# Optimization experiments

Measured on AMD Instinct MI355X. Metric: run time of the kernel, lower is better.

The kernel has to match this reference:

```python
import jax, jax.numpy as jnp
import numpy as np

L, N, D, DZ = 128, 65536, 8, 16


def setup_inputs() -> dict:
    key = jax.random.key(0)
    k1, k2, k3, k4 = jax.random.split(key, 4)
    y_true = jax.random.normal(k1, (N, D), dtype=jnp.float32)
    y_pred_array = jax.random.normal(k2, (L, N, D), dtype=jnp.float32)
    mu = jax.random.normal(k3, (N, DZ), dtype=jnp.float32)
    # Sigma must be positive (log(Sigma)); uniform in (eps, 1)
    Sigma = jax.random.uniform(k4, (N, DZ), dtype=jnp.float32, minval=1e-3, maxval=1.0)
    return {"y_true": y_true, "y_pred_array": y_pred_array, "mu": mu, "Sigma": Sigma}


def reference(y_true, y_pred_array, mu, Sigma):
    alpha = 1.0  # unused in alter=True branch
    Lsz = y_pred_array.shape[0]
    # per-n mean and covariance over the L sample axis (batched cov_3d)
    ymean = jnp.mean(y_pred_array, axis=0)              # (N, D)
    xc = y_pred_array - ymean[None, :, :]               # (L, N, D)
    ycov = jnp.einsum('lnd,lne->nde', xc, xc) / (Lsz - 1)  # (N, D, D)

    # KL term: mean_n of -(1 + log Sigma - mu^2 - Sigma).sum(-1) / 2
    KLloss = jnp.mean(-jnp.sum(1.0 + jnp.log(Sigma) - mu ** 2 - Sigma, axis=-1) / 2.0)

    # Reconstruction: mean_n of (log|det C_n| + m_n^T C_n^{-1} m_n) / 2
    m = ymean - y_true                                  # (N, D)
    _, logabsdet = jnp.linalg.slogdet(ycov)             # log|det| per n
    sol = jnp.linalg.solve(ycov, m[..., None])[..., 0]  # C^{-1} m, (N, D)
    quad = jnp.einsum('nd,nd->n', sol, m)
    Rec_loss = jnp.mean((logabsdet + quad) / 2.0)
    # original uses .data (detached) for Rec_loss
    Rec_loss = jax.lax.stop_gradient(Rec_loss)

    return (KLloss + Rec_loss, KLloss, Rec_loss)
```

## Files before the change

### kernel.cpp

```cpp
#include <hip/hip_runtime.h>
#include <math.h>

#define L_SAMP 128
#define N_TOT  65536
#define DIM    8
#define DZ_DIM 16
#define NTRI   (DIM*(DIM+1)/2)

__global__ __launch_bounds__(256, 1) void loss_main_kernel(
    const float* __restrict__ y_true,
    const float* __restrict__ y_pred,
    const float* __restrict__ mu,
    const float* __restrict__ Sigma,
    double* __restrict__ ws_acc)
{
    const int n = blockIdx.x * blockDim.x + threadIdx.x;

    float s[DIM];
    float p[NTRI];
#pragma unroll
    for (int d = 0; d < DIM; ++d) s[d] = 0.0f;
#pragma unroll
    for (int i = 0; i < NTRI; ++i) p[i] = 0.0f;

    const float4* base = reinterpret_cast<const float4*>(y_pred + (size_t)n * DIM);
    const size_t strideF4 = (size_t)N_TOT * DIM / 4;

#pragma unroll 4
    for (int l = 0; l < L_SAMP; ++l) {
        float4 a = base[(size_t)l * strideF4];
        float4 b = base[(size_t)l * strideF4 + 1];
        float y[DIM] = {a.x, a.y, a.z, a.w, b.x, b.y, b.z, b.w};
#pragma unroll
        for (int d = 0; d < DIM; ++d) s[d] += y[d];
        int idx = 0;
#pragma unroll
        for (int d = 0; d < DIM; ++d) {
#pragma unroll
            for (int e = d; e < DIM; ++e) {
                p[idx] += y[d] * y[e];
                ++idx;
            }
        }
    }

    float mean[DIM];
#pragma unroll
    for (int d = 0; d < DIM; ++d) mean[d] = s[d] * (1.0f / L_SAMP);

    float C[DIM][DIM];
    {
        int idx = 0;
#pragma unroll
        for (int d = 0; d < DIM; ++d) {
#pragma unroll
            for (int e = d; e < DIM; ++e) {
                float c = (p[idx] - (float)L_SAMP * mean[d] * mean[e]) * (1.0f / (L_SAMP - 1));
                C[d][e] = c;
                C[e][d] = c;
                ++idx;
            }
        }
    }

    const float4* yt = reinterpret_cast<const float4*>(y_true + (size_t)n * DIM);
    float4 t0 = yt[0];
    float4 t1 = yt[1];
    float m[DIM] = {mean[0] - t0.x, mean[1] - t0.y, mean[2] - t0.z, mean[3] - t0.w,
                    mean[4] - t1.x, mean[5] - t1.y, mean[6] - t1.z, mean[7] - t1.w};

    float G[DIM][DIM];
    float logdet = 0.0f;
#pragma unroll
    for (int k = 0; k < DIM; ++k) {
        float diag = C[k][k];
#pragma unroll
        for (int j = 0; j < DIM; ++j) {
            if (j < k) diag -= G[k][j] * G[k][j];
        }
        float gkk = sqrtf(diag);
        G[k][k] = gkk;
        logdet += logf(diag);
        float inv = 1.0f / gkk;
#pragma unroll
        for (int i = 0; i < DIM; ++i) {
            if (i > k) {
                float v = C[i][k];
#pragma unroll
                for (int j = 0; j < DIM; ++j) {
                    if (j < k) v -= G[i][j] * G[k][j];
                }
                G[i][k] = v * inv;
            }
        }
    }

    float z[DIM];
    float quad = 0.0f;
#pragma unroll
    for (int i = 0; i < DIM; ++i) {
        float v = m[i];
#pragma unroll
        for (int j = 0; j < DIM; ++j) {
            if (j < i) v -= G[i][j] * z[j];
        }
        z[i] = v / G[i][i];
        quad += z[i] * z[i];
    }
    float rec = 0.5f * (logdet + quad);

    const float4* muv = reinterpret_cast<const float4*>(mu + (size_t)n * DZ_DIM);
    const float4* sgv = reinterpret_cast<const float4*>(Sigma + (size_t)n * DZ_DIM);
    float kl = 0.0f;
#pragma unroll
    for (int j = 0; j < DZ_DIM / 4; ++j) {
        float4 mv = muv[j];
        float4 sv = sgv[j];
        kl += mv.x * mv.x + sv.x - logf(sv.x) - 1.0f;
        kl += mv.y * mv.y + sv.y - logf(sv.y) - 1.0f;
        kl += mv.z * mv.z + sv.z - logf(sv.z) - 1.0f;
        kl += mv.w * mv.w + sv.w - logf(sv.w) - 1.0f;
    }
    kl *= 0.5f;

    double dk = (double)kl;
    double dr = (double)rec;
#pragma unroll
    for (int off = 32; off > 0; off >>= 1) {
        dk += __shfl_down(dk, off);
        dr += __shfl_down(dr, off);
    }
    if ((threadIdx.x & 63) == 0) {
        atomicAdd(&ws_acc[0], dk);
        atomicAdd(&ws_acc[1], dr);
    }
}

__global__ void loss_finalize_kernel(const double* __restrict__ ws_acc,
                                     float* __restrict__ out)
{
    double kl  = ws_acc[0] / (double)N_TOT;
    double rec = ws_acc[1] / (double)N_TOT;
    out[0] = (float)(kl + rec);
    out[1] = (float)kl;
    out[2] = (float)rec;
}

extern "C" void kernel_launch(void* const* d_in, const int* in_sizes, int n_in,
                              void* d_out, int out_size, void* d_ws, size_t ws_size,
                              hipStream_t stream) {
    const float* y_true = (const float*)d_in[0];
    const float* y_pred = (const float*)d_in[1];
    const float* mu     = (const float*)d_in[2];
    const float* Sigma  = (const float*)d_in[3];
    float* out  = (float*)d_out;
    double* ws  = (double*)d_ws;

    hipMemsetAsync(ws, 0, 2 * sizeof(double), stream);

    loss_main_kernel<<<N_TOT / 256, 256, 0, stream>>>(y_true, y_pred, mu, Sigma, ws);
    loss_finalize_kernel<<<1, 1, 0, stream>>>(ws, out);
}
```

Baseline: 381.2 us.

## Split sample axis across four waves per block with LDS partial-sum reduction

Each block now handles 64 points, with its four waves each accumulating the sum and second-moment statistics over a quarter of the L samples. The partial sums go through LDS and are combined by wave 0, which then does the Cholesky, solve and KL work. The launch grows from 256 to 1024 blocks, giving more parallel memory streams to hide latency on a bandwidth-bound read of y_pred. In exchange it adds LDS traffic and a barrier, and three of the four waves sit idle during the serial Cholesky tail.

Result: no change. 381.1 us (-0.0%).

```diff
diff --git a/kernel.cpp b/kernel.cpp
--- a/kernel.cpp
+++ b/kernel.cpp
@@ -5,134 +5,156 @@
 #define N_TOT  65536
 #define DIM    8
 #define DZ_DIM 16
-#define NTRI   (DIM*(DIM+1)/2)
+#define NTRI   36
+#define NPB    64
+#define CHUNKS 4
+#define LPC    (L_SAMP / CHUNKS)
+#define LDSTR  45
 
-__global__ __launch_bounds__(256, 1) void loss_main_kernel(
+__host__ __device__ constexpr int tri(int d, int e) {
+    return d * DIM - d * (d - 1) / 2 + (e - d);
+}
+__host__ __device__ constexpr int gi(int i, int j) {
+    return i * (i + 1) / 2 + j;
+}
+
+__global__ __launch_bounds__(256, 4) void loss_main_kernel(
     const float* __restrict__ y_true,
     const float* __restrict__ y_pred,
     const float* __restrict__ mu,
     const float* __restrict__ Sigma,
     double* __restrict__ ws_acc)
 {
-    const int n = blockIdx.x * blockDim.x + threadIdx.x;
+    __shared__ float lds[(CHUNKS - 1) * NPB * LDSTR];
+
+    const int t = threadIdx.x;
+    const int i = t & 63;
+    const int c = t >> 6;
+    const int n = blockIdx.x * NPB + i;
 
     float s[DIM];
     float p[NTRI];
 #pragma unroll
     for (int d = 0; d < DIM; ++d) s[d] = 0.0f;
 #pragma unroll
-    for (int i = 0; i < NTRI; ++i) p[i] = 0.0f;
+    for (int j = 0; j < NTRI; ++j) p[j] = 0.0f;
 
-    const float4* base = reinterpret_cast<const float4*>(y_pred + (size_t)n * DIM);
-    const size_t strideF4 = (size_t)N_TOT * DIM / 4;
+    const float* src = y_pred + ((size_t)(c * LPC) * N_TOT + (size_t)n) * DIM;
+    const size_t strideF = (size_t)N_TOT * DIM;
 
-#pragma unroll 4
-    for (int l = 0; l < L_SAMP; ++l) {
-        float4 a = base[(size_t)l * strideF4];
-        float4 b = base[(size_t)l * strideF4 + 1];
+#pragma unroll 2
+    for (int l = 0; l < LPC; ++l) {
+        const float4* q = reinterpret_cast<const float4*>(src + (size_t)l * strideF);
+        float4 a = q[0];
+        float4 b = q[1];
         float y[DIM] = {a.x, a.y, a.z, a.w, b.x, b.y, b.z, b.w};
 #pragma unroll
         for (int d = 0; d < DIM; ++d) s[d] += y[d];
-        int idx = 0;
 #pragma unroll
-        for (int d = 0; d < DIM; ++d) {
+        for (int d = 0; d < DIM; ++d)
 #pragma unroll
-            for (int e = d; e < DIM; ++e) {
-                p[idx] += y[d] * y[e];
-                ++idx;
+            for (int e = d; e < DIM; ++e)
+                p[tri(d, e)] += y[d] * y[e];
+    }
+
+    if (c > 0) {
+        float* dst = &lds[((c - 1) * NPB + i) * LDSTR];
+#pragma unroll
+        for (int d = 0; d < DIM; ++d) dst[d] = s[d];
+#pragma unroll
+        for (int j = 0; j < NTRI; ++j) dst[DIM + j] = p[j];
+    }
+    __syncthreads();
+
+    if (c == 0) {
+#pragma unroll
+        for (int k = 0; k < CHUNKS - 1; ++k) {
+            const float* srcl = &lds[(k * NPB + i) * LDSTR];
+#pragma unroll
+            for (int d = 0; d < DIM; ++d) s[d] += srcl[d];
+#pragma unroll
+            for (int j = 0; j < NTRI; ++j) p[j] += srcl[DIM + j];
+        }
+
+        float mean[DIM];
+#pragma unroll
+        for (int d = 0; d < DIM; ++d) mean[d] = s[d] * (1.0f / L_SAMP);
+
+#pragma unroll
+        for (int d = 0; d < DIM; ++d)
+#pragma unroll
+            for (int e = d; e < DIM; ++e)
+                p[tri(d, e)] = (p[tri(d, e)] - (float)L_SAMP * mean[d] * mean[e])
+                               * (1.0f / (L_SAMP - 1));
+
+        const float4* yt = reinterpret_cast<const float4*>(y_true + (size_t)n * DIM);
+        float4 t0 = yt[0];
+        float4 t1 = yt[1];
+        float m[DIM] = {mean[0] - t0.x, mean[1] - t0.y, mean[2] - t0.z, mean[3] - t0.w,
+                        mean[4] - t1.x, mean[5] - t1.y, mean[6] - t1.z, mean[7] - t1.w};
+
+        float G[NTRI];
+        float logdet = 0.0f;
+#pragma unroll
+        for (int k = 0; k < DIM; ++k) {
+            float diag = p[tri(k, k)];
+#pragma unroll
+            for (int j = 0; j < DIM; ++j)
+                if (j < k) diag -= G[gi(k, j)] * G[gi(k, j)];
+            float gkk = sqrtf(diag);
+            G[gi(k, k)] = gkk;
+            logdet += logf(diag);
+            float inv = 1.0f / gkk;
+#pragma unroll
+            for (int r = 0; r < DIM; ++r) {
+                if (r > k) {
+                    float v = p[tri(k, r)];
+#pragma unroll
+                    for (int j = 0; j < DIM; ++j)
+                        if (j < k) v -= G[gi(r, j)] * G[gi(k, j)];
+                    G[gi(r, k)] = v * inv;
+                }
             }
         }
-    }
 
-    float mean[DIM];
+        float z[DIM];
+        float quad = 0.0f;
 #pragma unroll
-    for (int d = 0; d < DIM; ++d) mean[d] = s[d] * (1.0f / L_SAMP);
+        for (int r = 0; r < DIM; ++r) {
+            float v = m[r];
+#pragma unroll
+            for (int j = 0; j < DIM; ++j)
+                if (j < r) v -= G[gi(r, j)] * z[j];
+            z[r] = v / G[gi(r, r)];
+            quad += z[r] * z[r];
+        }
+        float rec = 0.5f * (logdet + quad);
 
-    float C[DIM][DIM];
-    {
-        int idx = 0;
+        const float4* muv = reinterpret_cast<const float4*>(mu + (size_t)n * DZ_DIM);
+        const float4* sgv = reinterpret_cast<const float4*>(Sigma + (size_t)n * DZ_DIM);
+        float kl = 0.0f;
 #pragma unroll
-        for (int d = 0; d < DIM; ++d) {
+        for (int j = 0; j < DZ_DIM / 4; ++j) {
+            float4 mv = muv[j];
+            float4 sv = sgv[j];
+            kl += mv.x * mv.x + sv.x - logf(sv.x) - 1.0f;
+            kl += mv.y * mv.y + sv.y - logf(sv.y) - 1.0f;
+            kl += mv.z * mv.z + sv.z - logf(sv.z) - 1.0f;
+            kl += mv.w * mv.w + sv.w - logf(sv.w) - 1.0f;
+        }
+        kl *= 0.5f;
+
+        double dk = (double)kl;
+        double dr = (double)rec;
 #pragma unroll
-            for (int e = d; e < DIM; ++e) {
-                float c = (p[idx] - (float)L_SAMP * mean[d] * mean[e]) * (1.0f / (L_SAMP - 1));
-                C[d][e] = c;
-                C[e][d] = c;
-                ++idx;
-            }
+        for (int off = 32; off > 0; off >>= 1) {
+            dk += __shfl_down(dk, off);
+            dr += __shfl_down(dr, off);
         }
-    }
-
-    const float4* yt = reinterpret_cast<const float4*>(y_true + (size_t)n * DIM);
-    float4 t0 = yt[0];
-    float4 t1 = yt[1];
-    float m[DIM] = {mean[0] - t0.x, mean[1] - t0.y, mean[2] - t0.z, mean[3] - t0.w,
-                    mean[4] - t1.x, mean[5] - t1.y, mean[6] - t1.z, mean[7] - t1.w};
-
-    float G[DIM][DIM];
-    float logdet = 0.0f;
-#pragma unroll
-    for (int k = 0; k < DIM; ++k) {
-        float diag = C[k][k];
-#pragma unroll
-        for (int j = 0; j < DIM; ++j) {
-            if (j < k) diag -= G[k][j] * G[k][j];
+        if (i == 0) {
+            atomicAdd(&ws_acc[0], dk);
+            atomicAdd(&ws_acc[1], dr);
         }
-        float gkk = sqrtf(diag);
-        G[k][k] = gkk;
-        logdet += logf(diag);
-        float inv = 1.0f / gkk;
-#pragma unroll
-        for (int i = 0; i < DIM; ++i) {
-            if (i > k) {
-                float v = C[i][k];
-#pragma unroll
-                for (int j = 0; j < DIM; ++j) {
-                    if (j < k) v -= G[i][j] * G[k][j];
-                }
-                G[i][k] = v * inv;
-            }
-        }
-    }
-
-    float z[DIM];
-    float quad = 0.0f;
-#pragma unroll
-    for (int i = 0; i < DIM; ++i) {
-        float v = m[i];
-#pragma unroll
-        for (int j = 0; j < DIM; ++j) {
-            if (j < i) v -= G[i][j] * z[j];
-        }
-        z[i] = v / G[i][i];
-        quad += z[i] * z[i];
-    }
-    float rec = 0.5f * (logdet + quad);
-
-    const float4* muv = reinterpret_cast<const float4*>(mu + (size_t)n * DZ_DIM);
-    const float4* sgv = reinterpret_cast<const float4*>(Sigma + (size_t)n * DZ_DIM);
-    float kl = 0.0f;
-#pragma unroll
-    for (int j = 0; j < DZ_DIM / 4; ++j) {
-        float4 mv = muv[j];
-        float4 sv = sgv[j];
-        kl += mv.x * mv.x + sv.x - logf(sv.x) - 1.0f;
-        kl += mv.y * mv.y + sv.y - logf(sv.y) - 1.0f;
-        kl += mv.z * mv.z + sv.z - logf(sv.z) - 1.0f;
-        kl += mv.w * mv.w + sv.w - logf(sv.w) - 1.0f;
-    }
-    kl *= 0.5f;
-
-    double dk = (double)kl;
-    double dr = (double)rec;
-#pragma unroll
-    for (int off = 32; off > 0; off >>= 1) {
-        dk += __shfl_down(dk, off);
-        dr += __shfl_down(dr, off);
-    }
-    if ((threadIdx.x & 63) == 0) {
-        atomicAdd(&ws_acc[0], dk);
-        atomicAdd(&ws_acc[1], dr);
     }
 }
 
@@ -158,6 +180,6 @@
 
     hipMemsetAsync(ws, 0, 2 * sizeof(double), stream);
 
-    loss_main_kernel<<<N_TOT / 256, 256, 0, stream>>>(y_true, y_pred, mu, Sigma, ws);
+    loss_main_kernel<<<N_TOT / NPB, 256, 0, stream>>>(y_true, y_pred, mu, Sigma, ws);
     loss_finalize_kernel<<<1, 1, 0, stream>>>(ws, out);
 }
```
